# Kernel tuning notes

Hardware: AMD Instinct MI355X
Metric: run time of the kernel (lower is better)

## Reference

```python
import jax, jax.numpy as jnp
import numpy as np

N = 500_000      # total observations
D = 40           # per-observation feature dim
S = 2048         # number of segments (time series)
WIDTH = 128      # psi hidden width
LATENT = 128     # latent width
DOT = 64         # dot_prod_dim
HEADS = 4        # n_heads


def setup_inputs() -> dict:
    key = jax.random.key(0)
    ks = jax.random.split(key, 12)

    def he(k, shape):
        fan_in = shape[0]
        lim = np.sqrt(6.0 / fan_in)
        return jax.random.uniform(k, shape, jnp.float32, -lim, lim)

    inputs = jax.random.normal(ks[0], (N, D), jnp.float32)
    segment_ids = jnp.sort(jax.random.randint(ks[1], (N,), 0, S))
    lengths = jax.random.randint(ks[2], (S,), 0, 300)
    return {
        "inputs": inputs,
        "segment_ids": segment_ids,
        "lengths": lengths,
        "W1": he(ks[3], (D, WIDTH)),      "b1": jnp.zeros((WIDTH,), jnp.float32),
        "W2": he(ks[4], (WIDTH, WIDTH)), "b2": jnp.zeros((WIDTH,), jnp.float32),
        "W3": he(ks[5], (WIDTH, LATENT)),"b3": jnp.zeros((LATENT,), jnp.float32),
        "Wr": he(ks[6], (LATENT, LATENT)),"br": jnp.zeros((LATENT,), jnp.float32),
        "W_k": he(ks[7], (LATENT + D, DOT * HEADS)),
        "W_q": jax.random.normal(ks[8], (HEADS, DOT), jnp.float32) * 0.02,
    }


def segment_softmax(x, seg, num_segments):
    # x: [N, H]; softmax over elements sharing the same segment id
    m = jax.ops.segment_max(x, seg, num_segments, indices_are_sorted=True)
    e = jnp.exp(x - m[seg])
    denom = jax.ops.segment_sum(e, seg, num_segments, indices_are_sorted=True)
    return e / denom[seg]


def reference(inputs, segment_ids, lengths, W1, b1, W2, b2, W3, b3, Wr, br, W_k, W_q):
    relu = jax.nn.relu
    # psi: 2 hidden dense layers + latent projection (all relu)
    h = relu(inputs @ W1 + b1)
    h = relu(h @ W2 + b2)
    enc = relu(h @ W3 + b3)                                   # [N, LATENT]
    # segment mean aggregation
    sums = jax.ops.segment_sum(enc, segment_ids, S, indices_are_sorted=True)
    counts = jax.ops.segment_sum(jnp.ones((enc.shape[0], 1), enc.dtype),
                                 segment_ids, S, indices_are_sorted=True)
    agg = sums / jnp.maximum(counts, 1.0)                      # [S, LATENT]
    agg = relu(agg @ Wr + br)                                  # rho
    # broadcast back and combine
    combined = jnp.concatenate([inputs, agg[segment_ids]], axis=-1)  # [N, D+LATENT]
    keys = (combined @ W_k).reshape(-1, HEADS, DOT)            # split+stack == reshape
    preattn = jnp.einsum('nhd,hd->nh', keys, W_q) / jnp.sqrt(jnp.float32(DOT))
    attn = segment_softmax(preattn, segment_ids, S)            # [N, H]
    # match original: list of per-head [N, 1] tensors -> stacked [H, N, 1]
    return jnp.transpose(attn)[..., None]
```

## Files before the change

kernel.cpp:

```cpp
#include <hip/hip_runtime.h>
#include <math.h>


#define NROWS 500000
#define DIM 40
#define NSEG 2048
#define DOTD 64
#define NH 4
#define BLOCK 256
#define SEG_PER_BLOCK 4
#define CACHE_IT 6

__global__ __launch_bounds__(BLOCK) void prep_kernel(
    const int* __restrict__ seg,
    const float* __restrict__ Wk,
    const float* __restrict__ Wq,
    int* __restrict__ seg_start,
    int* __restrict__ seg_end,
    float* __restrict__ wxg)
{
    const int tid = (int)threadIdx.x;
    const int n = (int)(blockIdx.x * BLOCK + tid);

    if (blockIdx.x == 0 && tid < DIM * NH) {
        const int d = tid >> 2;
        const int h = tid & 3;
        const float* wkp = Wk + d * (NH * DOTD) + h * DOTD;
        const float* wqp = Wq + h * DOTD;
        float acc = 0.f;
        #pragma unroll
        for (int j = 0; j < DOTD; ++j) acc += wkp[j] * wqp[j];
        wxg[tid] = acc * 0.125f;
    }

    if (n < NROWS) {
        const int s = seg[n];
        if (n == 0) {
            seg_start[s] = 0;
            for (int t = 0; t < s; ++t) { seg_start[t] = 0; seg_end[t] = 0; }
        } else {
            const int sp = seg[n - 1];
            if (sp != s) {
                seg_start[s] = n;
                seg_end[sp] = n;
                for (int t = sp + 1; t < s; ++t) { seg_start[t] = n; seg_end[t] = n; }
            }
        }
        if (n == NROWS - 1) {
            seg_end[s] = NROWS;
            for (int t = s + 1; t < NSEG; ++t) { seg_start[t] = NROWS; seg_end[t] = NROWS; }
        }
    }
}

__global__ __launch_bounds__(BLOCK) void seg_attn_kernel(
    const float* __restrict__ x,
    const int* __restrict__ seg_start,
    const int* __restrict__ seg_end,
    const float* __restrict__ wxg,
    float* __restrict__ out)
{
    __shared__ float wx[DIM][NH];

    const int tid = (int)threadIdx.x;
    if (tid < DIM * NH) wx[tid >> 2][tid & 3] = wxg[tid];
    __syncthreads();

    const int lane = tid & 63;
    const int s = (int)blockIdx.x * SEG_PER_BLOCK + (tid >> 6);
    const int start = seg_start[s];
    const int end = seg_end[s];
    const int rows = end - start;
    if (rows <= 0) return;
    const int iters = (rows + 63) >> 6;

    float cache[CACHE_IT][NH];
    float lmax[NH];
    #pragma unroll
    for (int h = 0; h < NH; ++h) lmax[h] = -3.0e38f;

    for (int it = 0; it < iters; ++it) {
        const int i = it * 64 + lane;
        if (i < rows) {
            const float4* xr = (const float4*)(x + (size_t)(start + i) * DIM);
            float acc[NH] = {0.f, 0.f, 0.f, 0.f};
            #pragma unroll
            for (int q = 0; q < DIM / 4; ++q) {
                const float4 v = xr[q];
                #pragma unroll
                for (int h = 0; h < NH; ++h) {
                    acc[h] += v.x * wx[4 * q + 0][h];
                    acc[h] += v.y * wx[4 * q + 1][h];
                    acc[h] += v.z * wx[4 * q + 2][h];
                    acc[h] += v.w * wx[4 * q + 3][h];
                }
            }
            #pragma unroll
            for (int h = 0; h < NH; ++h) {
                if (it < CACHE_IT) cache[it][h] = acc[h];
                lmax[h] = fmaxf(lmax[h], acc[h]);
            }
        }
    }

    float m[NH];
    #pragma unroll
    for (int h = 0; h < NH; ++h) {
        float v = lmax[h];
        #pragma unroll
        for (int off = 32; off > 0; off >>= 1) v = fmaxf(v, __shfl_xor(v, off, 64));
        m[h] = v;
    }

    float lsum[NH] = {0.f, 0.f, 0.f, 0.f};
    for (int it = 0; it < iters; ++it) {
        const int i = it * 64 + lane;
        if (i < rows) {
            float e[NH];
            if (it < CACHE_IT) {
                #pragma unroll
                for (int h = 0; h < NH; ++h) {
                    e[h] = __expf(cache[it][h] - m[h]);
                    cache[it][h] = e[h];
                }
            } else {
                const float4* xr = (const float4*)(x + (size_t)(start + i) * DIM);
                float acc[NH] = {0.f, 0.f, 0.f, 0.f};
                for (int q = 0; q < DIM / 4; ++q) {
                    const float4 v = xr[q];
                    for (int h = 0; h < NH; ++h) {
                        acc[h] += v.x * wx[4 * q + 0][h] + v.y * wx[4 * q + 1][h]
                                + v.z * wx[4 * q + 2][h] + v.w * wx[4 * q + 3][h];
                    }
                }
                for (int h = 0; h < NH; ++h) e[h] = __expf(acc[h] - m[h]);
            }
            #pragma unroll
            for (int h = 0; h < NH; ++h) lsum[h] += e[h];
        }
    }
    float rden[NH];
    #pragma unroll
    for (int h = 0; h < NH; ++h) {
        float v = lsum[h];
        #pragma unroll
        for (int off = 32; off > 0; off >>= 1) v += __shfl_xor(v, off, 64);
        rden[h] = 1.0f / v;
    }

    for (int it = 0; it < iters; ++it) {
        const int i = it * 64 + lane;
        if (i < rows) {
            float e[NH];
            if (it < CACHE_IT) {
                #pragma unroll
                for (int h = 0; h < NH; ++h) e[h] = cache[it][h];
            } else {
                const float4* xr = (const float4*)(x + (size_t)(start + i) * DIM);
                float acc[NH] = {0.f, 0.f, 0.f, 0.f};
                for (int q = 0; q < DIM / 4; ++q) {
                    const float4 v = xr[q];
                    for (int h = 0; h < NH; ++h) {
                        acc[h] += v.x * wx[4 * q + 0][h] + v.y * wx[4 * q + 1][h]
                                + v.z * wx[4 * q + 2][h] + v.w * wx[4 * q + 3][h];
                    }
                }
                for (int h = 0; h < NH; ++h) e[h] = __expf(acc[h] - m[h]);
            }
            const int n = start + i;
            #pragma unroll
            for (int h = 0; h < NH; ++h) {
                out[(size_t)h * NROWS + n] = e[h] * rden[h];
            }
        }
    }
}

extern "C" void kernel_launch(void* const* d_in, const int* in_sizes, int n_in,
                              void* d_out, int out_size, void* d_ws, size_t ws_size,
                              hipStream_t stream) {
    const float* x  = (const float*)d_in[0];
    const int* seg  = (const int*)d_in[1];
    const float* Wk = (const float*)d_in[11];
    const float* Wq = (const float*)d_in[12];
    float* out = (float*)d_out;

    int* seg_start = (int*)d_ws;
    int* seg_end   = seg_start + NSEG;
    float* wxg     = (float*)(seg_end + NSEG);

    hipLaunchKernelGGL(prep_kernel, dim3((NROWS + BLOCK - 1) / BLOCK), dim3(BLOCK),
                       0, stream, seg, Wk, Wq, seg_start, seg_end, wxg);
    hipLaunchKernelGGL(seg_attn_kernel, dim3(NSEG / SEG_PER_BLOCK), dim3(BLOCK),
                       0, stream, x, seg_start, seg_end, wxg, out);
}
```

Before: 142.6 us.

## Process each segment with a full block instead of one wave

```diff
diff --git a/kernel.cpp b/kernel.cpp
--- a/kernel.cpp
+++ b/kernel.cpp
@@ -8,8 +8,8 @@
 #define DOTD 64
 #define NH 4
 #define BLOCK 256
-#define SEG_PER_BLOCK 4
-#define CACHE_IT 6
+#define NWAVE (BLOCK / 64)
+#define CACHE_IT 2
 
 __global__ __launch_bounds__(BLOCK) void prep_kernel(
     const int* __restrict__ seg,
@@ -53,7 +53,26 @@
     }
 }
 
-__global__ __launch_bounds__(BLOCK) void seg_attn_kernel(
+__device__ __forceinline__ void compute_logits(
+    const float* __restrict__ x, int n, const float (*wx)[NH], float* acc)
+{
+    const float4* xr = (const float4*)(x + (size_t)n * DIM);
+    #pragma unroll
+    for (int h = 0; h < NH; ++h) acc[h] = 0.f;
+    #pragma unroll
+    for (int q = 0; q < DIM / 4; ++q) {
+        const float4 v = xr[q];
+        #pragma unroll
+        for (int h = 0; h < NH; ++h) {
+            acc[h] += v.x * wx[4 * q + 0][h];
+            acc[h] += v.y * wx[4 * q + 1][h];
+            acc[h] += v.z * wx[4 * q + 2][h];
+            acc[h] += v.w * wx[4 * q + 3][h];
+        }
+    }
+}
+
+__global__ __launch_bounds__(BLOCK, 8) void seg_attn_kernel(
     const float* __restrict__ x,
     const int* __restrict__ seg_start,
     const int* __restrict__ seg_end,
@@ -61,117 +80,120 @@
     float* __restrict__ out)
 {
     __shared__ float wx[DIM][NH];
+    __shared__ float red_max[NWAVE][NH];
+    __shared__ float red_sum[NWAVE][NH];
 
     const int tid = (int)threadIdx.x;
     if (tid < DIM * NH) wx[tid >> 2][tid & 3] = wxg[tid];
+
+    const int s = (int)blockIdx.x;
+    const int start = seg_start[s];
+    const int rows = seg_end[s] - start;
     __syncthreads();
+    if (rows <= 0) return;
 
     const int lane = tid & 63;
-    const int s = (int)blockIdx.x * SEG_PER_BLOCK + (tid >> 6);
-    const int start = seg_start[s];
-    const int end = seg_end[s];
-    const int rows = end - start;
-    if (rows <= 0) return;
-    const int iters = (rows + 63) >> 6;
+    const int wid = tid >> 6;
+    const int iters = (rows + BLOCK - 1) / BLOCK;
 
     float cache[CACHE_IT][NH];
     float lmax[NH];
     #pragma unroll
     for (int h = 0; h < NH; ++h) lmax[h] = -3.0e38f;
 
-    for (int it = 0; it < iters; ++it) {
-        const int i = it * 64 + lane;
-        if (i < rows) {
-            const float4* xr = (const float4*)(x + (size_t)(start + i) * DIM);
-            float acc[NH] = {0.f, 0.f, 0.f, 0.f};
-            #pragma unroll
-            for (int q = 0; q < DIM / 4; ++q) {
-                const float4 v = xr[q];
-                #pragma unroll
-                for (int h = 0; h < NH; ++h) {
-                    acc[h] += v.x * wx[4 * q + 0][h];
-                    acc[h] += v.y * wx[4 * q + 1][h];
-                    acc[h] += v.z * wx[4 * q + 2][h];
-                    acc[h] += v.w * wx[4 * q + 3][h];
-                }
-            }
+    #pragma unroll
+    for (int it = 0; it < CACHE_IT; ++it) {
+        const int i = it * BLOCK + tid;
+        if (i < rows) {
+            float acc[NH];
+            compute_logits(x, start + i, wx, acc);
             #pragma unroll
             for (int h = 0; h < NH; ++h) {
-                if (it < CACHE_IT) cache[it][h] = acc[h];
+                cache[it][h] = acc[h];
                 lmax[h] = fmaxf(lmax[h], acc[h]);
             }
         }
     }
-
-    float m[NH];
+    for (int it = CACHE_IT; it < iters; ++it) {
+        const int i = it * BLOCK + tid;
+        if (i < rows) {
+            float acc[NH];
+            compute_logits(x, start + i, wx, acc);
+            #pragma unroll
+            for (int h = 0; h < NH; ++h) lmax[h] = fmaxf(lmax[h], acc[h]);
+        }
+    }
+
     #pragma unroll
     for (int h = 0; h < NH; ++h) {
         float v = lmax[h];
         #pragma unroll
         for (int off = 32; off > 0; off >>= 1) v = fmaxf(v, __shfl_xor(v, off, 64));
-        m[h] = v;
-    }
+        if (lane == 0) red_max[wid][h] = v;
+    }
+    __syncthreads();
+    float m[NH];
+    #pragma unroll
+    for (int h = 0; h < NH; ++h)
+        m[h] = fmaxf(fmaxf(red_max[0][h], red_max[1][h]),
+                     fmaxf(red_max[2][h], red_max[3][h]));
 
     float lsum[NH] = {0.f, 0.f, 0.f, 0.f};
-    for (int it = 0; it < iters; ++it) {
-        const int i = it * 64 + lane;
-        if (i < rows) {
-            float e[NH];
-            if (it < CACHE_IT) {
-                #pragma unroll
-                for (int h = 0; h < NH; ++h) {
-                    e[h] = __expf(cache[it][h] - m[h]);
-                    cache[it][h] = e[h];
-                }
-            } else {
-                const float4* xr = (const float4*)(x + (size_t)(start + i) * DIM);
-                float acc[NH] = {0.f, 0.f, 0.f, 0.f};
-                for (int q = 0; q < DIM / 4; ++q) {
-                    const float4 v = xr[q];
-                    for (int h = 0; h < NH; ++h) {
-                        acc[h] += v.x * wx[4 * q + 0][h] + v.y * wx[4 * q + 1][h]
-                                + v.z * wx[4 * q + 2][h] + v.w * wx[4 * q + 3][h];
-                    }
-                }
-                for (int h = 0; h < NH; ++h) e[h] = __expf(acc[h] - m[h]);
+    #pragma unroll
+    for (int it = 0; it < CACHE_IT; ++it) {
+        const int i = it * BLOCK + tid;
+        if (i < rows) {
+            #pragma unroll
+            for (int h = 0; h < NH; ++h) {
+                const float e = __expf(cache[it][h] - m[h]);
+                cache[it][h] = e;
+                lsum[h] += e;
             }
-            #pragma unroll
-            for (int h = 0; h < NH; ++h) lsum[h] += e[h];
-        }
-    }
-    float rden[NH];
+        }
+    }
+    for (int it = CACHE_IT; it < iters; ++it) {
+        const int i = it * BLOCK + tid;
+        if (i < rows) {
+            float acc[NH];
+            compute_logits(x, start + i, wx, acc);
+            #pragma unroll
+            for (int h = 0; h < NH; ++h) lsum[h] += __expf(acc[h] - m[h]);
+        }
+    }
+
     #pragma unroll
     for (int h = 0; h < NH; ++h) {
         float v = lsum[h];
         #pragma unroll
         for (int off = 32; off > 0; off >>= 1) v += __shfl_xor(v, off, 64);
-        rden[h] = 1.0f / v;
-    }
-
-    for (int it = 0; it < iters; ++it) {
-        const int i = it * 64 + lane;
-        if (i < rows) {
-            float e[NH];
-            if (it < CACHE_IT) {
-                #pragma unroll
-                for (int h = 0; h < NH; ++h) e[h] = cache[it][h];
-            } else {
-                const float4* xr = (const float4*)(x + (size_t)(start + i) * DIM);
-                float acc[NH] = {0.f, 0.f, 0.f, 0.f};
-                for (int q = 0; q < DIM / 4; ++q) {
-                    const float4 v = xr[q];
-                    for (int h = 0; h < NH; ++h) {
-                        acc[h] += v.x * wx[4 * q + 0][h] + v.y * wx[4 * q + 1][h]
-                                + v.z * wx[4 * q + 2][h] + v.w * wx[4 * q + 3][h];
-                    }
-                }
-                for (int h = 0; h < NH; ++h) e[h] = __expf(acc[h] - m[h]);
-            }
+        if (lane == 0) red_sum[wid][h] = v;
+    }
+    __syncthreads();
+    float rden[NH];
+    #pragma unroll
+    for (int h = 0; h < NH; ++h)
+        rden[h] = 1.0f / (red_sum[0][h] + red_sum[1][h] +
+                          red_sum[2][h] + red_sum[3][h]);
+
+    #pragma unroll
+    for (int it = 0; it < CACHE_IT; ++it) {
+        const int i = it * BLOCK + tid;
+        if (i < rows) {
             const int n = start + i;
             #pragma unroll
-            for (int h = 0; h < NH; ++h) {
-                out[(size_t)h * NROWS + n] = e[h] * rden[h];
-            }
+            for (int h = 0; h < NH; ++h)
+                out[(size_t)h * NROWS + n] = cache[it][h] * rden[h];
+        }
+    }
+    for (int it = CACHE_IT; it < iters; ++it) {
+        const int i = it * BLOCK + tid;
+        if (i < rows) {
+            float acc[NH];
+            compute_logits(x, start + i, wx, acc);
+            const int n = start + i;
+            #pragma unroll
+            for (int h = 0; h < NH; ++h)
+                out[(size_t)h * NROWS + n] = __expf(acc[h] - m[h]) * rden[h];
         }
     }
 }
@@ -191,6 +213,6 @@
 
     hipLaunchKernelGGL(prep_kernel, dim3((NROWS + BLOCK - 1) / BLOCK), dim3(BLOCK),
                        0, stream, seg, Wk, Wq, seg_start, seg_end, wxg);
-    hipLaunchKernelGGL(seg_attn_kernel, dim3(NSEG / SEG_PER_BLOCK), dim3(BLOCK),
+    hipLaunchKernelGGL(seg_attn_kernel, dim3(NSEG), dim3(BLOCK),
                        0, stream, x, seg_start, seg_end, wxg, out);
 }
```

Measured after the change: 255.6 us. +79.2%, slower.
